# Kernel optimization log

Hardware: AMD Instinct MI355X
Metric: run time of the kernel (lower is better)

## Reference

```python
import jax, jax.numpy as jnp
import numpy as np

N, E, B = 100_000, 1_000_000, 16
H = 16  # hidden width from layers=(16,16,1)


def setup_inputs() -> dict:
    key = jax.random.key(0)
    ks = iter(jax.random.split(key, 40))
    def randn(shape):
        return jax.random.normal(next(ks), shape, dtype=jnp.float32)
    def w(shape):
        fan_in = shape[0]
        return randn(shape) / np.sqrt(fan_in)
    inp = {
        'x': randn((N, 1)),
        'e': randn((E, 1)),
        'g': randn((B, 1)),
        # encoder: independent MLPs on raw 1-dim features
        'We_enc': w((1, H)), 'be_enc': jnp.zeros((H,), jnp.float32),
        'Wx_enc': w((1, H)), 'bx_enc': jnp.zeros((H,), jnp.float32),
        'Wg_enc': w((1, 1)), 'bg_enc': jnp.zeros((1,), jnp.float32),
        # core: edge in = 32(e)+32(src)+32(dst)+2(g)=98; node in = 32+16+2=50; global in = 2+16+16=34
        'We_core': w((98, H)), 'be_core': jnp.zeros((H,), jnp.float32),
        'Wx_core': w((50, H)), 'bx_core': jnp.zeros((H,), jnp.float32),
        'Wg_core': w((34, 1)), 'bg_core': jnp.zeros((1,), jnp.float32),
        # decoder: independent MLPs
        'We_dec': w((H, H)), 'be_dec': jnp.zeros((H,), jnp.float32),
        'Wx_dec': w((H, H)), 'bx_dec': jnp.zeros((H,), jnp.float32),
        'Wg_dec': w((1, 1)), 'bg_dec': jnp.zeros((1,), jnp.float32),
        # output transform: plain Linear
        'We_out': w((H, 2)), 'be_out': jnp.zeros((2,), jnp.float32),
        'Wx_out': w((H, 2)), 'bx_out': jnp.zeros((2,), jnp.float32),
        'Wg_out': w((1, 1)), 'bg_out': jnp.zeros((1,), jnp.float32),
        'edges': jax.random.randint(next(ks), (2, E), 0, N),
        'node_idx': jnp.sort(jax.random.randint(next(ks), (N,), 0, B)),
        'edge_idx': jnp.sort(jax.random.randint(next(ks), (E,), 0, B)),
        'steps': 2,
    }
    return inp


def reference(x, e, g,
              We_enc, be_enc, Wx_enc, bx_enc, Wg_enc, bg_enc,
              We_core, be_core, Wx_core, bx_core, Wg_core, bg_core,
              We_dec, be_dec, Wx_dec, bx_dec, Wg_dec, bg_dec,
              We_out, be_out, Wx_out, bx_out, Wg_out, bg_out,
              edges, node_idx, edge_idx, steps):
    relu = jax.nn.relu
    src, dst = edges[0], edges[1]

    # ---- encoder (independent blocks) ----
    e1 = relu(e @ We_enc + be_enc)   # [E,16]
    x1 = relu(x @ Wx_enc + bx_enc)   # [N,16]
    g1 = relu(g @ Wg_enc + bg_enc)   # [B,1]
    ec, xc, gc = e1, x1, g1

    # per-dst edge counts for scatter-mean
    counts = jax.ops.segment_sum(jnp.ones((e.shape[0], 1), jnp.float32), dst, num_segments=N)
    counts = jnp.maximum(counts, 1.0)

    outs_e, outs_x, outs_g = [], [], []
    for _ in range(steps):
        # concat latent0 with current latent
        e_in = jnp.concatenate([e1, ec], axis=1)  # [E,32]
        x_in = jnp.concatenate([x1, xc], axis=1)  # [N,32]
        g_in = jnp.concatenate([g1, gc], axis=1)  # [B,2]

        # ---- core ----
        # edge block: gather src/dst nodes and per-edge globals
        e_feat = jnp.concatenate([e_in, x_in[src], x_in[dst], g_in[edge_idx]], axis=1)  # [E,98]
        e_new = relu(e_feat @ We_core + be_core)  # [E,16]
        # node block: mean-aggregate new edges onto destination nodes
        agg_e = jax.ops.segment_sum(e_new, dst, num_segments=N) / counts  # [N,16]
        x_feat = jnp.concatenate([x_in, agg_e, g_in[node_idx]], axis=1)   # [N,50]
        x_new = relu(x_feat @ Wx_core + bx_core)  # [N,16]
        # global block: add-aggregate nodes and edges per graph
        node_agg = jax.ops.segment_sum(x_new, node_idx, num_segments=B)   # [B,16]
        edge_agg = jax.ops.segment_sum(e_new, edge_idx, num_segments=B)   # [B,16]
        g_feat = jnp.concatenate([g_in, node_agg, edge_agg], axis=1)      # [B,34]
        g_new = relu(g_feat @ Wg_core + bg_core)  # [B,1]
        ec, xc, gc = e_new, x_new, g_new

        # ---- decoder (independent) ----
        ed = relu(ec @ We_dec + be_dec)
        xd = relu(xc @ Wx_dec + bx_dec)
        gd = relu(gc @ Wg_dec + bg_dec)

        # ---- output transform (plain linear) ----
        outs_e.append(ed @ We_out + be_out)  # [E,2]
        outs_x.append(xd @ Wx_out + bx_out)  # [N,2]
        outs_g.append(gd @ Wg_out + bg_out)  # [B,1]

    return (jnp.stack(outs_e), jnp.stack(outs_x), jnp.stack(outs_g))
```

## Files before the change

### kernel.cpp

```cpp
#include <hip/hip_runtime.h>

#define DEV __device__ __forceinline__

DEV float relu(float v) { return v > 0.f ? v : 0.f; }

#define G1_OFF 0
#define GIN_OFF 16
#define WEE 48
#define BEE 64
#define WC  80
#define BC  1648
#define WD  1664
#define BD  1920
#define WO  1936
#define BO  1968
#define WXE 1972
#define BXE 1988
#define WXC 2004
#define BXC 2804
#define WXD 2820
#define BXD 3076
#define WXO 3092
#define BXO 3124
#define WGE 3126
#define BGE 3127
#define WGC 3128
#define BGC 3162
#define WGD 3163
#define BGD 3164
#define WGO 3165
#define BGO 3166
#define SMALL_N 3200

struct P {
    const float *x, *e, *g;
    const int *src, *dst, *nidx, *eidx;
    float *ec, *xin, *small, *eagg_rep, *nagg_rep;
    int *cnt, *rowptr, *cursor, *colidx;
    float *eperm;
    int *spk;
    int *dstperm;
    float *out;
    int N, E, B;
};

struct WIn {
    const float *we_enc, *be_enc, *wx_enc, *bx_enc, *wg_enc, *bg_enc;
    const float *wc, *bc, *wxc, *bxc, *wgc, *bgc;
    const float *wd, *bd, *wxd, *bxd, *wgd, *bgd;
    const float *wo, *bo, *wxo, *bxo, *wgo, *bgo;
};

__global__ __launch_bounds__(256) void k_init_small(P p, WIn w) {
    int t = threadIdx.x;
    float* S = p.small;
#define CP(ptr, off, len) for (int i = t; i < (len); i += 256) S[(off) + i] = ptr[i];
    CP(w.we_enc, WEE, 16) CP(w.be_enc, BEE, 16)
    CP(w.wc, WC, 1568)    CP(w.bc, BC, 16)
    CP(w.wd, WD, 256)     CP(w.bd, BD, 16)
    CP(w.wo, WO, 32)      CP(w.bo, BO, 2)
    CP(w.wx_enc, WXE, 16) CP(w.bx_enc, BXE, 16)
    CP(w.wxc, WXC, 800)   CP(w.bxc, BXC, 16)
    CP(w.wxd, WXD, 256)   CP(w.bxd, BXD, 16)
    CP(w.wxo, WXO, 32)    CP(w.bxo, BXO, 2)
    CP(w.wgc, WGC, 34)
#undef CP
    if (t == 0) {
        S[WGE] = w.wg_enc[0]; S[BGE] = w.bg_enc[0];
        S[BGC] = w.bgc[0];
        S[WGD] = w.wgd[0];    S[BGD] = w.bgd[0];
        S[WGO] = w.wgo[0];    S[BGO] = w.bgo[0];
    }
    if (t < p.B) {
        float gv = p.g[t];
        float g1 = relu(gv * w.wg_enc[0] + w.bg_enc[0]);
        S[G1_OFF + t] = g1;
        S[GIN_OFF + 2 * t] = g1;
        S[GIN_OFF + 2 * t + 1] = g1;
    }
    for (int r = t; r < 16 * 256; r += 256) p.nagg_rep[r] = 0.f;
    for (int r = t; r < 64 * 256; r += 256) p.eagg_rep[r] = 0.f;
}

__global__ __launch_bounds__(256) void k_init_nodes(P p, WIn w) {
    size_t n = (size_t)blockIdx.x * 256 + threadIdx.x;
    if (n >= (size_t)p.N) return;
    p.cnt[n] = 0;
    float xv = p.x[n];
    float* row = p.xin + n * 32;
#pragma unroll
    for (int h = 0; h < 16; h++) {
        float v = relu(xv * w.wx_enc[h] + w.bx_enc[h]);
        row[h] = v;
        row[16 + h] = v;
    }
}

__global__ __launch_bounds__(256) void k_hist(P p) {
    size_t i = (size_t)blockIdx.x * 256 + threadIdx.x;
    if (i >= (size_t)p.E) return;
    atomicAdd(&p.cnt[p.dst[i]], 1);
}

#define SCAN_T 1024
#define SCAN_V 4
__global__ __launch_bounds__(SCAN_T) void k_scan(P p) {
    __shared__ int wsum[16];
    __shared__ int carry_s;
    int t = threadIdx.x;
    int lane = t & 63, wid = t >> 6;
    if (t == 0) carry_s = 0;
    __syncthreads();
    int chunk = SCAN_T * SCAN_V;
    int nchunk = (p.N + chunk - 1) / chunk;
    for (int c = 0; c < nchunk; c++) {
        int base = c * chunk + t * SCAN_V;
        int v[SCAN_V];
        int s = 0;
#pragma unroll
        for (int k = 0; k < SCAN_V; k++) {
            int idx = base + k;
            v[k] = (idx < p.N) ? p.cnt[idx] : 0;
            s += v[k];
        }
        int incl = s;
#pragma unroll
        for (int off = 1; off < 64; off <<= 1) {
            int u = __shfl_up(incl, off);
            if (lane >= off) incl += u;
        }
        if (lane == 63) wsum[wid] = incl;
        __syncthreads();
        if (wid == 0) {
            int ws = (lane < 16) ? wsum[lane] : 0;
            int wincl = ws;
#pragma unroll
            for (int off = 1; off < 16; off <<= 1) {
                int u = __shfl_up(wincl, off);
                if (lane >= off) wincl += u;
            }
            if (lane < 16) wsum[lane] = wincl - ws;
        }
        __syncthreads();
        int carry = carry_s;
        int excl = carry + wsum[wid] + incl - s;
        int run = excl;
#pragma unroll
        for (int k = 0; k < SCAN_V; k++) {
            int idx = base + k;
            if (idx < p.N) { p.rowptr[idx] = run; p.cursor[idx] = run; }
            run += v[k];
        }
        __syncthreads();
        if (t == SCAN_T - 1) carry_s = excl + s;
        __syncthreads();
    }
    if (t == 0) p.rowptr[p.N] = carry_s;
}

__global__ __launch_bounds__(256) void k_scatter(P p) {
    size_t i = (size_t)blockIdx.x * 256 + threadIdx.x;
    if (i >= (size_t)p.E) return;
    int d = p.dst[i];
    int slot = atomicAdd(&p.cursor[d], 1);
    p.colidx[slot] = (int)i;
}

__global__ __launch_bounds__(256) void k_permute(P p) {
    size_t j = (size_t)blockIdx.x * 256 + threadIdx.x;
    if (j >= (size_t)p.E) return;
    int i = p.colidx[j];
    p.eperm[j] = p.e[i];
    p.spk[j] = p.src[i] | (p.eidx[i] << 24);
    p.dstperm[j] = p.dst[i];
}

template <int STEP0>
__global__ __launch_bounds__(256) void k_edge(P p, int s) {
    __shared__ float eagg_lds[16 * 17];
    const int t = threadIdx.x;
    for (int r = t; r < 16 * 17; r += 256) eagg_lds[r] = 0.f;
    __syncthreads();
    const size_t j = (size_t)blockIdx.x * 256 + t;
    const float* __restrict__ S = p.small;
    if (j < (size_t)p.E) {
        float acc[16];
#pragma unroll
        for (int h = 0; h < 16; h++) acc[h] = S[BC + h];
        float ev = p.eperm[j];
        unsigned sp = (unsigned)p.spk[j];
        int si = (int)(sp & 0xFFFFFFu);
        int b = (int)(sp >> 24);
        int di = p.dstperm[j];
        float e1v[16];
#pragma unroll
        for (int h = 0; h < 16; h++) e1v[h] = relu(ev * S[WEE + h] + S[BEE + h]);
#pragma unroll
        for (int jj = 0; jj < 16; jj++)
#pragma unroll
            for (int h = 0; h < 16; h++) acc[h] += e1v[jj] * S[WC + jj * 16 + h];
        if (STEP0) {
#pragma unroll
            for (int jj = 0; jj < 16; jj++)
#pragma unroll
                for (int h = 0; h < 16; h++) acc[h] += e1v[jj] * S[WC + (16 + jj) * 16 + h];
        } else {
            const float4* ecv = (const float4*)(p.ec + j * 16);
#pragma unroll
            for (int c = 0; c < 4; c++) {
                float4 v = ecv[c];
                float vv[4] = {v.x, v.y, v.z, v.w};
#pragma unroll
                for (int k = 0; k < 4; k++)
#pragma unroll
                    for (int h = 0; h < 16; h++) acc[h] += vv[k] * S[WC + (16 + c * 4 + k) * 16 + h];
            }
        }
        const float4* xs = (const float4*)(p.xin + (size_t)si * 32);
#pragma unroll
        for (int c = 0; c < 8; c++) {
            float4 v = xs[c];
            float vv[4] = {v.x, v.y, v.z, v.w};
#pragma unroll
            for (int k = 0; k < 4; k++)
#pragma unroll
                for (int h = 0; h < 16; h++) acc[h] += vv[k] * S[WC + (32 + c * 4 + k) * 16 + h];
        }
        const float4* xd = (const float4*)(p.xin + (size_t)di * 32);
#pragma unroll
        for (int c = 0; c < 8; c++) {
            float4 v = xd[c];
            float vv[4] = {v.x, v.y, v.z, v.w};
#pragma unroll
            for (int k = 0; k < 4; k++)
#pragma unroll
                for (int h = 0; h < 16; h++) acc[h] += vv[k] * S[WC + (64 + c * 4 + k) * 16 + h];
        }
        float g0 = S[GIN_OFF + 2 * b], gcv = S[GIN_OFF + 2 * b + 1];
#pragma unroll
        for (int h = 0; h < 16; h++) acc[h] += g0 * S[WC + 96 * 16 + h] + gcv * S[WC + 97 * 16 + h];
        float enew[16];
#pragma unroll
        for (int h = 0; h < 16; h++) enew[h] = relu(acc[h]);
        float4* eco = (float4*)(p.ec + j * 16);
#pragma unroll
        for (int c = 0; c < 4; c++)
            eco[c] = make_float4(enew[c * 4], enew[c * 4 + 1], enew[c * 4 + 2], enew[c * 4 + 3]);
#pragma unroll
        for (int h = 0; h < 16; h++) atomicAdd(&eagg_lds[b * 17 + h], enew[h]);
        int i = p.colidx[j];
        float d[16];
#pragma unroll
        for (int h2 = 0; h2 < 16; h2++) d[h2] = S[BD + h2];
#pragma unroll
        for (int h = 0; h < 16; h++)
#pragma unroll
            for (int h2 = 0; h2 < 16; h2++) d[h2] += enew[h] * S[WD + h * 16 + h2];
        float o0 = S[BO], o1 = S[BO + 1];
#pragma unroll
        for (int h2 = 0; h2 < 16; h2++) {
            float dv = relu(d[h2]);
            o0 += dv * S[WO + h2 * 2];
            o1 += dv * S[WO + h2 * 2 + 1];
        }
        ((float2*)p.out)[(size_t)s * p.E + i] = make_float2(o0, o1);
    }
    __syncthreads();
    {
        float v = eagg_lds[(t >> 4) * 17 + (t & 15)];
        if (v != 0.f)
            atomicAdd(p.eagg_rep + (size_t)(blockIdx.x & 63) * 256 + t, v);
    }
}

__global__ __launch_bounds__(256) void k_node(P p, int s) {
    const size_t n = (size_t)blockIdx.x * 256 + threadIdx.x;
    const bool valid = n < (size_t)p.N;
    const float* __restrict__ S = p.small;
    float xnew[16];
    int b = 0;
    if (valid) {
        float acc[16];
#pragma unroll
        for (int h = 0; h < 16; h++) acc[h] = S[BXC + h];
        float xv = p.x[n];
        float x1v[16];
#pragma unroll
        for (int h = 0; h < 16; h++) x1v[h] = relu(xv * S[WXE + h] + S[BXE + h]);
#pragma unroll
        for (int jj = 0; jj < 16; jj++)
#pragma unroll
            for (int h = 0; h < 16; h++) acc[h] += x1v[jj] * S[WXC + jj * 16 + h];
        const float4* xcv = (const float4*)(p.xin + n * 32 + 16);
#pragma unroll
        for (int c = 0; c < 4; c++) {
            float4 v = xcv[c];
            float vv[4] = {v.x, v.y, v.z, v.w};
#pragma unroll
            for (int k = 0; k < 4; k++)
#pragma unroll
                for (int h = 0; h < 16; h++) acc[h] += vv[k] * S[WXC + (16 + c * 4 + k) * 16 + h];
        }
        int start = p.rowptr[n], end = p.rowptr[n + 1];
        int cnt = end - start;
        float inv = (cnt > 0) ? 1.f / (float)cnt : 1.f;
        float sum[16];
#pragma unroll
        for (int k = 0; k < 16; k++) sum[k] = 0.f;
        for (int jj = start; jj < end; jj++) {
            const float4* er = (const float4*)(p.ec + (size_t)jj * 16);
            float4 a = er[0], b4 = er[1], c4 = er[2], d4 = er[3];
            sum[0] += a.x;  sum[1] += a.y;  sum[2] += a.z;  sum[3] += a.w;
            sum[4] += b4.x; sum[5] += b4.y; sum[6] += b4.z; sum[7] += b4.w;
            sum[8] += c4.x; sum[9] += c4.y; sum[10] += c4.z; sum[11] += c4.w;
            sum[12] += d4.x; sum[13] += d4.y; sum[14] += d4.z; sum[15] += d4.w;
        }
#pragma unroll
        for (int k = 0; k < 16; k++) {
            float av = sum[k] * inv;
#pragma unroll
            for (int h = 0; h < 16; h++) acc[h] += av * S[WXC + (32 + k) * 16 + h];
        }
        b = p.nidx[n];
        float g0 = S[GIN_OFF + 2 * b], gcv = S[GIN_OFF + 2 * b + 1];
#pragma unroll
        for (int h = 0; h < 16; h++) acc[h] += g0 * S[WXC + 48 * 16 + h] + gcv * S[WXC + 49 * 16 + h];
#pragma unroll
        for (int h = 0; h < 16; h++) xnew[h] = relu(acc[h]);
        float4* xo = (float4*)(p.xin + n * 32 + 16);
#pragma unroll
        for (int c = 0; c < 4; c++)
            xo[c] = make_float4(xnew[c * 4], xnew[c * 4 + 1], xnew[c * 4 + 2], xnew[c * 4 + 3]);
        float d[16];
#pragma unroll
        for (int h2 = 0; h2 < 16; h2++) d[h2] = S[BXD + h2];
#pragma unroll
        for (int h = 0; h < 16; h++)
#pragma unroll
            for (int h2 = 0; h2 < 16; h2++) d[h2] += xnew[h] * S[WXD + h * 16 + h2];
        float o0 = S[BXO], o1 = S[BXO + 1];
#pragma unroll
        for (int h2 = 0; h2 < 16; h2++) {
            float dv = relu(d[h2]);
            o0 += dv * S[WXO + h2 * 2];
            o1 += dv * S[WXO + h2 * 2 + 1];
        }
        ((float2*)p.out)[(size_t)2 * p.E + (size_t)s * p.N + n] = make_float2(o0, o1);
    } else {
#pragma unroll
        for (int h = 0; h < 16; h++) xnew[h] = 0.f;
    }
    int b0 = __shfl(b, 0);
    bool uni = __all(!valid || b == b0);
    float* rep = p.nagg_rep + (size_t)(blockIdx.x & 15) * 256;
    if (uni) {
#pragma unroll
        for (int h = 0; h < 16; h++) {
            float v = xnew[h];
            v += __shfl_down(v, 32); v += __shfl_down(v, 16); v += __shfl_down(v, 8);
            v += __shfl_down(v, 4);  v += __shfl_down(v, 2);  v += __shfl_down(v, 1);
            if ((threadIdx.x & 63) == 0) atomicAdd(rep + b0 * 16 + h, v);
        }
    } else if (valid) {
#pragma unroll
        for (int h = 0; h < 16; h++) atomicAdd(rep + b * 16 + h, xnew[h]);
    }
}

__global__ __launch_bounds__(256) void k_global(P p, int s) {
    __shared__ float na[256], ea[256];
    int t = threadIdx.x;
    float sn = 0.f, se = 0.f;
    for (int r = 0; r < 16; r++) sn += p.nagg_rep[r * 256 + t];
    for (int r = 0; r < 64; r++) se += p.eagg_rep[r * 256 + t];
    na[t] = sn;
    ea[t] = se;
    __syncthreads();
    if (t < p.B) {
        const float* S = p.small;
        float g0 = S[GIN_OFF + 2 * t], gcv = S[GIN_OFF + 2 * t + 1];
        float acc = S[BGC] + g0 * S[WGC + 0] + gcv * S[WGC + 1];
#pragma unroll
        for (int h = 0; h < 16; h++) acc += na[t * 16 + h] * S[WGC + 2 + h];
#pragma unroll
        for (int h = 0; h < 16; h++) acc += ea[t * 16 + h] * S[WGC + 18 + h];
        float gn = relu(acc);
        p.small[GIN_OFF + 2 * t + 1] = gn;
        float gd = relu(gn * S[WGD] + S[BGD]);
        float og = gd * S[WGO] + S[BGO];
        p.out[(size_t)4 * p.E + (size_t)4 * p.N + (size_t)s * p.B + t] = og;
    }
    __syncthreads();
    for (int r = t; r < 16 * 256; r += 256) p.nagg_rep[r] = 0.f;
    for (int r = t; r < 64 * 256; r += 256) p.eagg_rep[r] = 0.f;
}

extern "C" void kernel_launch(void* const* d_in, const int* in_sizes, int n_in,
                              void* d_out, int out_size, void* d_ws, size_t ws_size,
                              hipStream_t stream) {
    int N = in_sizes[0], E = in_sizes[1], B = in_sizes[2];
    P p;
    p.x = (const float*)d_in[0];
    p.e = (const float*)d_in[1];
    p.g = (const float*)d_in[2];
    const int* edges = (const int*)d_in[27];
    p.src = edges;
    p.dst = edges + E;
    p.nidx = (const int*)d_in[28];
    p.eidx = (const int*)d_in[29];

    float* ws = (float*)d_ws;
    size_t off = 0;
    p.ec = ws + off;        off += (size_t)E * 16;
    p.xin = ws + off;       off += (size_t)N * 32;
    p.eagg_rep = ws + off;  off += 64 * 256;
    p.nagg_rep = ws + off;  off += 16 * 256;
    p.small = ws + off;     off += SMALL_N;
    p.cnt = (int*)(ws + off);     off += N;
    p.rowptr = (int*)(ws + off);  off += (size_t)N + 1;
    p.cursor = (int*)(ws + off);  off += N;
    p.colidx = (int*)(ws + off);  off += E;
    p.eperm = ws + off;           off += E;
    p.spk = (int*)(ws + off);     off += E;
    p.dstperm = (int*)(ws + off); off += E;
    p.out = (float*)d_out;
    p.N = N; p.E = E; p.B = B;

    WIn w;
    w.we_enc = (const float*)d_in[3];  w.be_enc = (const float*)d_in[4];
    w.wx_enc = (const float*)d_in[5];  w.bx_enc = (const float*)d_in[6];
    w.wg_enc = (const float*)d_in[7];  w.bg_enc = (const float*)d_in[8];
    w.wc = (const float*)d_in[9];      w.bc = (const float*)d_in[10];
    w.wxc = (const float*)d_in[11];    w.bxc = (const float*)d_in[12];
    w.wgc = (const float*)d_in[13];    w.bgc = (const float*)d_in[14];
    w.wd = (const float*)d_in[15];     w.bd = (const float*)d_in[16];
    w.wxd = (const float*)d_in[17];    w.bxd = (const float*)d_in[18];
    w.wgd = (const float*)d_in[19];    w.bgd = (const float*)d_in[20];
    w.wo = (const float*)d_in[21];     w.bo = (const float*)d_in[22];
    w.wxo = (const float*)d_in[23];    w.bxo = (const float*)d_in[24];
    w.wgo = (const float*)d_in[25];    w.bgo = (const float*)d_in[26];

    int nb = (N + 255) / 256, eb = (E + 255) / 256;
    k_init_small<<<1, 256, 0, stream>>>(p, w);
    k_init_nodes<<<nb, 256, 0, stream>>>(p, w);
    k_hist<<<eb, 256, 0, stream>>>(p);
    k_scan<<<1, SCAN_T, 0, stream>>>(p);
    k_scatter<<<eb, 256, 0, stream>>>(p);
    k_permute<<<eb, 256, 0, stream>>>(p);
    for (int s = 0; s < 2; s++) {
        if (s == 0) k_edge<1><<<eb, 256, 0, stream>>>(p, s);
        else        k_edge<0><<<eb, 256, 0, stream>>>(p, s);
        k_node<<<nb, 256, 0, stream>>>(p, s);
        k_global<<<1, 256, 0, stream>>>(p, s);
    }
}
```

Measured before the change: 826.9 us.

## Fuse per-node edge aggregation into edge kernel and merge scatter with permute

Moves the mean-aggregation of new edge features from the node kernel, which re-read ec in CSR order, into the edge kernel. Each block segment-reduces runs of equal destination in LDS and writes or atomically adds them into a per-node agg buffer. The node kernel reads and clears that buffer. The scatter and permute kernels are merged into one build kernel, and step 1 skips writing ec. This cuts global traffic on the 64 MB edge feature array, at the cost of extra LDS (about 17 KB per block), a serial per-run loop and float atomics that make summation order nondeterministic.

```diff
diff --git a/kernel.cpp b/kernel.cpp
--- a/kernel.cpp
+++ b/kernel.cpp
@@ -35,8 +35,8 @@
 struct P {
     const float *x, *e, *g;
     const int *src, *dst, *nidx, *eidx;
-    float *ec, *xin, *small, *eagg_rep, *nagg_rep;
-    int *cnt, *rowptr, *cursor, *colidx;
+    float *ec, *xin, *agg, *small, *eagg_rep, *nagg_rep;
+    int *cnt, *rowptr, *cursor, *origidx;
     float *eperm;
     int *spk;
     int *dstperm;
@@ -94,6 +94,10 @@
         row[h] = v;
         row[16 + h] = v;
     }
+    float4 z = make_float4(0.f, 0.f, 0.f, 0.f);
+    float4* a = (float4*)(p.agg + n * 16);
+#pragma unroll
+    for (int c = 0; c < 4; c++) a[c] = z;
 }
 
 __global__ __launch_bounds__(256) void k_hist(P p) {
@@ -158,32 +162,33 @@
     if (t == 0) p.rowptr[p.N] = carry_s;
 }
 
-__global__ __launch_bounds__(256) void k_scatter(P p) {
+__global__ __launch_bounds__(256) void k_build(P p) {
     size_t i = (size_t)blockIdx.x * 256 + threadIdx.x;
     if (i >= (size_t)p.E) return;
     int d = p.dst[i];
     int slot = atomicAdd(&p.cursor[d], 1);
-    p.colidx[slot] = (int)i;
-}
-
-__global__ __launch_bounds__(256) void k_permute(P p) {
-    size_t j = (size_t)blockIdx.x * 256 + threadIdx.x;
-    if (j >= (size_t)p.E) return;
-    int i = p.colidx[j];
-    p.eperm[j] = p.e[i];
-    p.spk[j] = p.src[i] | (p.eidx[i] << 24);
-    p.dstperm[j] = p.dst[i];
-}
-
-template <int STEP0>
+    p.eperm[slot] = p.e[i];
+    p.spk[slot] = p.src[i] | (p.eidx[i] << 24);
+    p.dstperm[slot] = d;
+    p.origidx[slot] = (int)i;
+}
+
+template <int STEP0, int SAVE_EC>
 __global__ __launch_bounds__(256) void k_edge(P p, int s) {
     __shared__ float eagg_lds[16 * 17];
+    __shared__ float sagg[256][16];
+    __shared__ int sd[256];
     const int t = threadIdx.x;
     for (int r = t; r < 16 * 17; r += 256) eagg_lds[r] = 0.f;
     __syncthreads();
     const size_t j = (size_t)blockIdx.x * 256 + t;
     const float* __restrict__ S = p.small;
-    if (j < (size_t)p.E) {
+    float enew[16];
+#pragma unroll
+    for (int h = 0; h < 16; h++) enew[h] = 0.f;
+    int di = -1;
+    const bool valid = j < (size_t)p.E;
+    if (valid) {
         float acc[16];
 #pragma unroll
         for (int h = 0; h < 16; h++) acc[h] = S[BC + h];
@@ -191,7 +196,7 @@
         unsigned sp = (unsigned)p.spk[j];
         int si = (int)(sp & 0xFFFFFFu);
         int b = (int)(sp >> 24);
-        int di = p.dstperm[j];
+        di = p.dstperm[j];
         float e1v[16];
 #pragma unroll
         for (int h = 0; h < 16; h++) e1v[h] = relu(ev * S[WEE + h] + S[BEE + h]);
@@ -239,16 +244,17 @@
         float g0 = S[GIN_OFF + 2 * b], gcv = S[GIN_OFF + 2 * b + 1];
 #pragma unroll
         for (int h = 0; h < 16; h++) acc[h] += g0 * S[WC + 96 * 16 + h] + gcv * S[WC + 97 * 16 + h];
-        float enew[16];
 #pragma unroll
         for (int h = 0; h < 16; h++) enew[h] = relu(acc[h]);
-        float4* eco = (float4*)(p.ec + j * 16);
-#pragma unroll
-        for (int c = 0; c < 4; c++)
-            eco[c] = make_float4(enew[c * 4], enew[c * 4 + 1], enew[c * 4 + 2], enew[c * 4 + 3]);
+        if (SAVE_EC) {
+            float4* eco = (float4*)(p.ec + j * 16);
+#pragma unroll
+            for (int c = 0; c < 4; c++)
+                eco[c] = make_float4(enew[c * 4], enew[c * 4 + 1], enew[c * 4 + 2], enew[c * 4 + 3]);
+        }
 #pragma unroll
         for (int h = 0; h < 16; h++) atomicAdd(&eagg_lds[b * 17 + h], enew[h]);
-        int i = p.colidx[j];
+        int i = p.origidx[j];
         float d[16];
 #pragma unroll
         for (int h2 = 0; h2 < 16; h2++) d[h2] = S[BD + h2];
@@ -265,7 +271,31 @@
         }
         ((float2*)p.out)[(size_t)s * p.E + i] = make_float2(o0, o1);
     }
+    sd[t] = di;
+#pragma unroll
+    for (int h = 0; h < 16; h++) sagg[t][h] = enew[h];
     __syncthreads();
+    if (valid && (t == 0 || sd[t - 1] != di)) {
+        float sum[16];
+#pragma unroll
+        for (int h = 0; h < 16; h++) sum[h] = sagg[t][h];
+        int k = t + 1;
+        while (k < 256 && sd[k] == di) {
+#pragma unroll
+            for (int h = 0; h < 16; h++) sum[h] += sagg[k][h];
+            k++;
+        }
+        size_t jend = j + (size_t)(k - t);
+        int rs = p.rowptr[di], re = p.rowptr[di + 1];
+        float* arow = p.agg + (size_t)di * 16;
+        if (j == (size_t)rs && jend == (size_t)re) {
+#pragma unroll
+            for (int h = 0; h < 16; h++) arow[h] = sum[h];
+        } else {
+#pragma unroll
+            for (int h = 0; h < 16; h++) atomicAdd(arow + h, sum[h]);
+        }
+    }
     {
         float v = eagg_lds[(t >> 4) * 17 + (t & 15)];
         if (v != 0.f)
@@ -301,25 +331,20 @@
 #pragma unroll
                 for (int h = 0; h < 16; h++) acc[h] += vv[k] * S[WXC + (16 + c * 4 + k) * 16 + h];
         }
-        int start = p.rowptr[n], end = p.rowptr[n + 1];
-        int cnt = end - start;
+        int cnt = p.rowptr[n + 1] - p.rowptr[n];
         float inv = (cnt > 0) ? 1.f / (float)cnt : 1.f;
-        float sum[16];
-#pragma unroll
-        for (int k = 0; k < 16; k++) sum[k] = 0.f;
-        for (int jj = start; jj < end; jj++) {
-            const float4* er = (const float4*)(p.ec + (size_t)jj * 16);
-            float4 a = er[0], b4 = er[1], c4 = er[2], d4 = er[3];
-            sum[0] += a.x;  sum[1] += a.y;  sum[2] += a.z;  sum[3] += a.w;
-            sum[4] += b4.x; sum[5] += b4.y; sum[6] += b4.z; sum[7] += b4.w;
-            sum[8] += c4.x; sum[9] += c4.y; sum[10] += c4.z; sum[11] += c4.w;
-            sum[12] += d4.x; sum[13] += d4.y; sum[14] += d4.z; sum[15] += d4.w;
-        }
-#pragma unroll
-        for (int k = 0; k < 16; k++) {
-            float av = sum[k] * inv;
-#pragma unroll
-            for (int h = 0; h < 16; h++) acc[h] += av * S[WXC + (32 + k) * 16 + h];
+        float4* arow = (float4*)(p.agg + n * 16);
+#pragma unroll
+        for (int c = 0; c < 4; c++) {
+            float4 v = arow[c];
+            float vv[4] = {v.x, v.y, v.z, v.w};
+#pragma unroll
+            for (int k = 0; k < 4; k++) {
+                float av = vv[k] * inv;
+#pragma unroll
+                for (int h = 0; h < 16; h++) acc[h] += av * S[WXC + (32 + c * 4 + k) * 16 + h];
+            }
+            arow[c] = make_float4(0.f, 0.f, 0.f, 0.f);
         }
         b = p.nidx[n];
         float g0 = S[GIN_OFF + 2 * b], gcv = S[GIN_OFF + 2 * b + 1];
@@ -413,13 +438,14 @@
     size_t off = 0;
     p.ec = ws + off;        off += (size_t)E * 16;
     p.xin = ws + off;       off += (size_t)N * 32;
+    p.agg = ws + off;       off += (size_t)N * 16;
     p.eagg_rep = ws + off;  off += 64 * 256;
     p.nagg_rep = ws + off;  off += 16 * 256;
     p.small = ws + off;     off += SMALL_N;
     p.cnt = (int*)(ws + off);     off += N;
     p.rowptr = (int*)(ws + off);  off += (size_t)N + 1;
     p.cursor = (int*)(ws + off);  off += N;
-    p.colidx = (int*)(ws + off);  off += E;
+    p.origidx = (int*)(ws + off); off += E;
     p.eperm = ws + off;           off += E;
     p.spk = (int*)(ws + off);     off += E;
     p.dstperm = (int*)(ws + off); off += E;
@@ -445,11 +471,10 @@
     k_init_nodes<<<nb, 256, 0, stream>>>(p, w);
     k_hist<<<eb, 256, 0, stream>>>(p);
     k_scan<<<1, SCAN_T, 0, stream>>>(p);
-    k_scatter<<<eb, 256, 0, stream>>>(p);
-    k_permute<<<eb, 256, 0, stream>>>(p);
+    k_build<<<eb, 256, 0, stream>>>(p);
     for (int s = 0; s < 2; s++) {
-        if (s == 0) k_edge<1><<<eb, 256, 0, stream>>>(p, s);
-        else        k_edge<0><<<eb, 256, 0, stream>>>(p, s);
+        if (s == 0) k_edge<1, 1><<<eb, 256, 0, stream>>>(p, s);
+        else        k_edge<0, 0><<<eb, 256, 0, stream>>>(p, s);
         k_node<<<nb, 256, 0, stream>>>(p, s);
         k_global<<<1, 256, 0, stream>>>(p, s);
     }
```

After: 797.3 us. 3.6% less time.
